# Kernel tuning notes

Hardware: AMD Instinct MI355X
Metric: run time of the kernel (lower is better)

## Reference

```python
import jax, jax.numpy as jnp
import numpy as np

DELTA = 0.1
LRELU_SLOPE = 0.01
BN_EPS = 1e-5


def ternarize(t, d):
    # {-1, 0, +1}: 0 where |t| < d, sign(t) otherwise (matches the torch where-chain)
    return jnp.where(jnp.abs(t) < d, 0.0, jnp.sign(t))


def ste_ternarize(t, d):
    # straight-through estimator, matching the torch .data-swap trick
    return t + jax.lax.stop_gradient(ternarize(t, d) - t)


def conv2d(x, w, stride, pad):
    return jax.lax.conv_general_dilated(
        x, w, (stride, stride), [(pad, pad), (pad, pad)],
        dimension_numbers=('NCHW', 'OIHW', 'NCHW'))


def batchnorm(x, gamma, beta, mean, var):
    inv = gamma / jnp.sqrt(var + BN_EPS)
    return x * inv[None, :, None, None] + (beta - mean * inv)[None, :, None, None]


def lrelu(x):
    return jnp.where(x > 0, x, LRELU_SLOPE * x)


def setup_inputs() -> dict:
    key = jax.random.key(0)
    ks = jax.random.split(key, 12)
    B, Cin, C, H, W = 16, 32, 64, 256, 256
    return {
        'x':      jax.random.normal(ks[0], (B, Cin, H, W), jnp.float32),
        'w11':    jax.random.normal(ks[1], (C, Cin, 3, 3), jnp.float32),
        'b11':    jax.random.normal(ks[2], (C,), jnp.float32),
        'w1':     jax.random.normal(ks[3], (C, Cin, 3, 3), jnp.float32),
        'b1':     jax.random.normal(ks[4], (C,), jnp.float32),
        'w2':     jax.random.normal(ks[5], (C, C, 3, 3), jnp.float32),
        'b2':     jax.random.normal(ks[6], (C,), jnp.float32),
        'gamma_p': jax.random.uniform(ks[7], (Cin,), jnp.float32),
        'beta_p':  jax.random.normal(ks[8], (Cin,), jnp.float32),
        'mean_p':  jax.random.normal(ks[9], (Cin,), jnp.float32),
        'var_p':   jnp.ones((Cin,), jnp.float32),
        'gamma1':  jax.random.uniform(ks[10], (C,), jnp.float32),
        'beta1':   jax.random.normal(ks[11], (C,), jnp.float32),
        'mean1':   jax.random.normal(jax.random.fold_in(key, 99), (C,), jnp.float32),
        'var1':    jnp.ones((C,), jnp.float32),
    }


def reference(x, w11, b11, w1, b1, w2, b2,
              gamma_p, beta_p, mean_p, var_p,
              gamma1, beta1, mean1, var1):
    # shortcut conv11 (stride 3); NOTE: torch mutates input.data in-place, so
    # the main branch below consumes the x already ternarized with d11.
    d11 = DELTA * jnp.max(jnp.abs(w11))
    x_t = ste_ternarize(x, d11)
    prev_mp = conv2d(x_t, ste_ternarize(w11, d11), 3, 1) \
        + ste_ternarize(b11, d11)[None, :, None, None]

    # main branch: pre_bn -> lrelu -> conv1 (stride 1) -> bn1 -> lrelu -> dropout(eval) -> conv2 (stride 3)
    out = lrelu(batchnorm(x_t, gamma_p, beta_p, mean_p, var_p))

    d1 = DELTA * jnp.max(jnp.abs(w1))
    out = conv2d(ste_ternarize(out, d1), ste_ternarize(w1, d1), 1, 1) \
        + ste_ternarize(b1, d1)[None, :, None, None]
    out = lrelu(batchnorm(out, gamma1, beta1, mean1, var1))
    # dropout: identity in eval mode

    d2 = DELTA * jnp.max(jnp.abs(w2))
    out = conv2d(ste_ternarize(out, d2), ste_ternarize(w2, d2), 3, 1) \
        + ste_ternarize(b2, d2)[None, :, None, None]

    return lrelu(out + prev_mp)  # [16, 64, 86, 86]
```

## Files before the change

kernel.cpp:

```cpp
#include <hip/hip_runtime.h>
#include <stdint.h>

#define B 16
#define CIN 32
#define C 64
#define H 256
#define W 256
#define OH 86
#define OW 86
#define PIX (OH*OW)
#define PADW 272
#define PWORDS (PADW*PADW*8)

typedef int v4i __attribute__((ext_vector_type(4)));

#define OFF_D      0
#define OFF_MAPW   64
#define OFF_B11    768
#define OFF_B2     1280
#define OFF_TLO    1536
#define OFF_THI    1792
#define OFF_W11R   4096
#define OFF_W1R    24576
#define OFF_W2R    45056
#define OFF_XTP    262144
#define OFF_XMAP   38141952

__device__ __forceinline__ int tern_i(float t, float d) {
    return (fabsf(t) < d) ? 0 : (t > 0.f ? 1 : -1);
}

__global__ __launch_bounds__(1024) void k_absmax(const float* w11, const float* w1,
                                                 const float* w2, unsigned* dws) {
    __shared__ unsigned red[1024];
    int b = blockIdx.x;
    const float* p = (b == 0) ? w11 : (b == 1) ? w1 : w2;
    int n = (b == 2) ? 36864 : 18432;
    unsigned m = 0;
    for (int i = threadIdx.x; i < n; i += 1024)
        m = max(m, __float_as_uint(fabsf(p[i])));
    red[threadIdx.x] = m; __syncthreads();
    for (int s = 512; s > 0; s >>= 1) {
        if (threadIdx.x < s) red[threadIdx.x] = max(red[threadIdx.x], red[threadIdx.x + s]);
        __syncthreads();
    }
    if (threadIdx.x == 0) dws[b] = red[0];
}

__global__ __launch_bounds__(256) void k_prep(const float* w11, const float* w1, const float* w2,
                                              const float* b11, const float* b1, const float* b2,
                                              const float* gp, const float* bp, const float* mp, const float* vp,
                                              const float* g1, const float* be1, const float* me1, const float* v1,
                                              char* ws) {
    const unsigned* dw = (const unsigned*)(ws + OFF_D);
    float d11 = __fmul_rn(0.1f, __uint_as_float(dw[0]));
    float d1  = __fmul_rn(0.1f, __uint_as_float(dw[1]));
    float d2v = __fmul_rn(0.1f, __uint_as_float(dw[2]));
    int idx = blockIdx.x * 256 + threadIdx.x;
    if (idx < 4608) {
        int j = idx & 3, c16 = (idx >> 2) & 15, cot = (idx >> 6) & 3;
        int q1 = (idx >> 8) & 1, pos = idx >> 9;
        int co = cot * 16 + c16;
        unsigned wd = 0;
        #pragma unroll
        for (int jj = 0; jj < 4; jj++) {
            int ci = q1 * 16 + j * 4 + jj;
            int tv = tern_i(w1[(co * 32 + ci) * 9 + pos], d1);
            wd |= ((unsigned)(tv & 255)) << (8 * jj);
        }
        ((int*)(ws + OFF_W1R))[idx] = (int)wd;
    } else if (idx < 9216) {
        int i2 = idx - 4608;
        int j = i2 & 3, c16 = (i2 >> 2) & 15, cot = (i2 >> 6) & 3;
        int q1 = (i2 >> 8) & 1, pos = i2 >> 9;
        int co = cot * 16 + c16;
        unsigned wd = 0;
        #pragma unroll
        for (int jj = 0; jj < 4; jj++) {
            int ci = q1 * 16 + j * 4 + jj;
            int tv = tern_i(w11[(co * 32 + ci) * 9 + pos], d11);
            wd |= ((unsigned)(tv & 255)) << (8 * jj);
        }
        ((int*)(ws + OFF_W11R))[i2] = (int)wd;
    } else if (idx < 18432) {
        int i2 = idx - 9216;
        int j = i2 & 3, q = (i2 >> 2) & 3, c16 = (i2 >> 4) & 15;
        int cot = (i2 >> 8) & 3, pos = i2 >> 10;
        int co = cot * 16 + c16;
        unsigned wd = 0;
        #pragma unroll
        for (int jj = 0; jj < 4; jj++) {
            int ci = q * 16 + j * 4 + jj;
            int tv = tern_i(w2[(co * 64 + ci) * 9 + pos], d2v);
            wd |= ((unsigned)(tv & 255)) << (8 * jj);
        }
        ((int*)(ws + OFF_W2R))[i2] = (int)wd;
    } else {
        int i = idx - 18432;
        if (i < 64) {
            ((int*)(ws + OFF_B11))[i] = tern_i(b11[i], d11);
        } else if (i < 128) {
            ((int*)(ws + OFF_B2))[i - 64] = tern_i(b2[i - 64], d2v);
        } else if (i < 152) {
            int j = i - 128;
            int g = j / 3, s = j % 3;
            float v = (float)(s - 1);
            unsigned wd = 0;
            #pragma unroll
            for (int jj = 0; jj < 4; jj++) {
                int c = g * 4 + jj;
                float inv = __fdiv_rn(gp[c], __fsqrt_rn(__fadd_rn(vp[c], 1e-5f)));
                float sh  = __fsub_rn(bp[c], __fmul_rn(mp[c], inv));
                float z   = __fadd_rn(__fmul_rn(v, inv), sh);
                z = (z > 0.f) ? z : __fmul_rn(0.01f, z);
                wd |= ((unsigned)(tern_i(z, d1) & 255)) << (8 * jj);
            }
            ((int*)(ws + OFF_MAPW))[j] = (int)wd;
        } else if (i < 216) {
            int co = i - 152;
            float inv = __fdiv_rn(g1[co], __fsqrt_rn(__fadd_rn(v1[co], 1e-5f)));
            float sh  = __fsub_rn(be1[co], __fmul_rn(me1[co], inv));
            int lo = 1000, hi = 1000;
            for (int vi = -290; vi <= 290; ++vi) {
                float z = __fadd_rn(__fmul_rn((float)vi, inv), sh);
                z = (z > 0.f) ? z : __fmul_rn(0.01f, z);
                int cls = (fabsf(z) < d2v) ? 0 : (z > 0.f ? 1 : -1);
                if (cls >= 0 && lo == 1000) lo = vi;
                if (cls == 1 && hi == 1000) hi = vi;
            }
            int b1t = tern_i(b1[co], d1);
            ((int*)(ws + OFF_TLO))[co] = lo - b1t;
            ((int*)(ws + OFF_THI))[co] = hi - b1t;
        }
    }
}

__global__ __launch_bounds__(256) void k_tern_x(const float* __restrict__ x,
                                                char* __restrict__ ws) {
    int bidx = blockIdx.x;
    if (bidx >= 4096) {
        int idx = (bidx - 4096) * 256 + threadIdx.x;
        int n = idx / 8448, c = idx - n * 8448;
        int row, col;
        if (c < 4352) {
            int r = c / 272; col = c - r * 272; row = (r < 2) ? r : r + 256;
        } else {
            int c2 = c - 4352; int k = c2 & 15;
            row = 2 + (c2 >> 4); col = (k < 2) ? k : k + 256;
        }
        size_t base = ((size_t)n * (PADW * PADW) + (size_t)row * PADW + col) * 2;
        int4 z = make_int4(0, 0, 0, 0);
        ((int4*)(ws + OFF_XTP))[base] = z;  ((int4*)(ws + OFF_XTP))[base + 1] = z;
        ((int4*)(ws + OFF_XMAP))[base] = z; ((int4*)(ws + OFF_XMAP))[base + 1] = z;
        return;
    }
    float d11 = __fmul_rn(0.1f, __uint_as_float(((const unsigned*)(ws + OFF_D))[0]));
    const int* mapw = (const int*)(ws + OFF_MAPW);
    int idx = bidx * 256 + threadIdx.x;
    int pix = idx & 65535, n = idx >> 16;
    int y = pix >> 8, xq = pix & 255;
    const float* xp = x + ((size_t)n * CIN << 16) + pix;
    int rw[8], mw[8];
    #pragma unroll
    for (int g = 0; g < 8; ++g) {
        unsigned Wn = (unsigned)mapw[g * 3 + 0];
        unsigned W0 = (unsigned)mapw[g * 3 + 1];
        unsigned Wp = (unsigned)mapw[g * 3 + 2];
        unsigned r = 0;
        #pragma unroll
        for (int j = 0; j < 4; ++j) {
            float v = xp[(size_t)(g * 4 + j) << 16];
            int tv = tern_i(v, d11);
            r |= ((unsigned)(tv & 255)) << (8 * j);
        }
        unsigned nb = (r & 0x80808080u) >> 7;
        unsigned pb = (r & 0x01010101u) & ~nb;
        unsigned nm = nb * 0xFFu, pm = pb * 0xFFu;
        unsigned zm = ~(nm | pm);
        rw[g] = (int)r;
        mw[g] = (int)((Wn & nm) | (W0 & zm) | (Wp & pm));
    }
    size_t base = ((size_t)n * (PADW * PADW) + (size_t)(y + 2) * PADW + (xq + 2)) * 2;
    int4* o1 = (int4*)(ws + OFF_XTP) + base;
    o1[0] = make_int4(rw[0], rw[1], rw[2], rw[3]);
    o1[1] = make_int4(rw[4], rw[5], rw[6], rw[7]);
    int4* o2 = (int4*)(ws + OFF_XMAP) + base;
    o2[0] = make_int4(mw[0], mw[1], mw[2], mw[3]);
    o2[1] = make_int4(mw[4], mw[5], mw[6], mw[7]);
}

__global__ __launch_bounds__(256, 3) void k_net(const char* __restrict__ ws,
                                                float* __restrict__ out) {
    __shared__ int t2L[576 * 16];
    int tid = threadIdx.x, bid = blockIdx.x;
    int tx = bid % 11; int tt = bid / 11; int ty = tt % 11; int n = tt / 11;
    int OH0 = ty * 8, OW0 = tx * 8;
    int Y0 = OH0 * 3 - 2, X0 = OW0 * 3 - 2;
    int c16 = tid & 15, q = (tid >> 4) & 3, wv = tid >> 6;
    int q1 = q & 1, qh = q >> 1;
    const int* xmapn = (const int*)(ws + OFF_XMAP) + (size_t)n * PWORDS;
    const int* xtpn  = (const int*)(ws + OFF_XTP)  + (size_t)n * PWORDS;

    const int* w1r = (const int*)(ws + OFF_W1R);
    v4i bw1[5][4];
    #pragma unroll
    for (int c = 0; c < 5; ++c) {
        int pos = 2 * c + qh;
        #pragma unroll
        for (int ct = 0; ct < 4; ++ct) {
            v4i z = {0, 0, 0, 0};
            if (pos < 9) z = *(const v4i*)&w1r[((pos * 2 + q1) * 4 + ct) * 64 + c16 * 4];
            bw1[c][ct] = z;
        }
    }
    const int* TLO = (const int*)(ws + OFF_TLO);
    const int* THI = (const int*)(ws + OFF_THI);
    v4i tlo4[4], thi4[4];
    #pragma unroll
    for (int ct = 0; ct < 4; ++ct) {
        tlo4[ct] = *(const v4i*)&TLO[ct * 16 + q * 4];
        thi4[ct] = *(const v4i*)&THI[ct * 16 + q * 4];
    }

    int Yb = Y0 + 2, Xb = X0 + 2;
    #pragma unroll 1
    for (int pg = 0; pg < 9; ++pg) {
        int pbase = (wv * 9 + pg) * 16;
        int fp = pbase + c16;
        int iy = fp / 24, ix = fp - iy * 24;
        v4i a[5];
        #pragma unroll
        for (int c = 0; c < 5; ++c) {
            int pos = 2 * c + qh;
            v4i z = {0, 0, 0, 0};
            if (pos < 9) {
                int kh = pos / 3, kw = pos - kh * 3;
                z = *(const v4i*)&xmapn[((Yb + iy + kh) * PADW + (Xb + ix + kw)) * 8 + q1 * 4];
            }
            a[c] = z;
        }
        bool wok = ((unsigned)(Y0 + 1 + iy) < H) && ((unsigned)(X0 + 1 + ix) < W);
        int key = (fp >> 1) & 3;
        #pragma unroll
        for (int ct = 0; ct < 4; ++ct) {
            v4i acc = {0, 0, 0, 0};
            #pragma unroll
            for (int c = 0; c < 5; ++c)
                acc = __builtin_amdgcn_mfma_i32_16x16x64_i8(bw1[c][ct], a[c], acc, 0, 0, 0);
            unsigned wcol = 0;
            #pragma unroll
            for (int i = 0; i < 4; ++i) {
                int cls = (acc[i] >= tlo4[ct][i] ? 1 : 0) + (acc[i] >= thi4[ct][i] ? 1 : 0) - 1;
                wcol |= ((unsigned)(cls & 255)) << (8 * i);
            }
            t2L[fp * 16 + ((ct ^ key) << 2) + q] = wok ? (int)wcol : 0;
        }
    }

    int o = wv * 16 + c16;
    int oh8 = o >> 3, ow8 = o & 7;
    int gOH = OH0 + oh8, gOW = OW0 + ow8;
    v4i a11[5];
    #pragma unroll
    for (int c = 0; c < 5; ++c) {
        int pos = 2 * c + qh;
        v4i z = {0, 0, 0, 0};
        if (pos < 9) {
            int kh = pos / 3, kw = pos - kh * 3;
            int ih = gOH * 3 - 1 + kh, iw = gOW * 3 - 1 + kw;
            z = *(const v4i*)&xtpn[((ih + 2) * PADW + (iw + 2)) * 8 + q1 * 4];
        }
        a11[c] = z;
    }
    const int* w11r = (const int*)(ws + OFF_W11R);
    v4i acc11[4];
    #pragma unroll
    for (int ct = 0; ct < 4; ++ct) {
        v4i acc1 = {0, 0, 0, 0};
        #pragma unroll
        for (int c = 0; c < 5; ++c) {
            int pos = 2 * c + qh;
            v4i b = {0, 0, 0, 0};
            if (pos < 9) b = *(const v4i*)&w11r[((pos * 2 + q1) * 4 + ct) * 64 + c16 * 4];
            acc1 = __builtin_amdgcn_mfma_i32_16x16x64_i8(a11[c], b, acc1, 0, 0, 0);
        }
        acc11[ct] = acc1;
    }
    __syncthreads();

    v4i a2[9];
    #pragma unroll
    for (int pos = 0; pos < 9; ++pos) {
        int kh = pos / 3, kw = pos - kh * 3;
        int p2 = (oh8 * 3 + kh) * 24 + ow8 * 3 + kw;
        int g2 = q ^ ((p2 >> 1) & 3);
        a2[pos] = *(const v4i*)&t2L[p2 * 16 + g2 * 4];
    }
    const int* w2r = (const int*)(ws + OFF_W2R);
    v4i acc2[4];
    #pragma unroll
    for (int ct = 0; ct < 4; ++ct) {
        v4i acc = {0, 0, 0, 0};
        #pragma unroll
        for (int pos = 0; pos < 9; ++pos) {
            v4i b = *(const v4i*)&w2r[((pos * 4 + ct) * 16 + c16) * 16 + q * 4];
            acc = __builtin_amdgcn_mfma_i32_16x16x64_i8(a2[pos], b, acc, 0, 0, 0);
        }
        acc2[ct] = acc;
    }

    const int* b2i = (const int*)(ws + OFF_B2);
    const int* b11i = (const int*)(ws + OFF_B11);
    int pt0 = wv * 16 + q * 4;
    int ohh = OH0 + (pt0 >> 3);
    int oww = OW0 + (pt0 & 7);
    if (ohh < OH) {
        #pragma unroll
        for (int ct = 0; ct < 4; ++ct) {
            int co = ct * 16 + c16;
            int bc = b2i[co] + b11i[co];
            float f[4];
            #pragma unroll
            for (int i = 0; i < 4; ++i) {
                float z = (float)(acc2[ct][i] + acc11[ct][i] + bc);
                f[i] = (z > 0.f) ? z : __fmul_rn(0.01f, z);
            }
            float* op = out + ((size_t)(n * 64 + co)) * PIX + ohh * OW + oww;
            if (oww + 3 < OW) {
                *(float4*)op = make_float4(f[0], f[1], f[2], f[3]);
            } else {
                #pragma unroll
                for (int i = 0; i < 4; ++i)
                    if (oww + i < OW) op[i] = f[i];
            }
        }
    }
}

extern "C" void kernel_launch(void* const* d_in, const int* in_sizes, int n_in,
                              void* d_out, int out_size, void* d_ws, size_t ws_size,
                              hipStream_t stream) {
    const float* x    = (const float*)d_in[0];
    const float* w11  = (const float*)d_in[1];
    const float* b11  = (const float*)d_in[2];
    const float* w1   = (const float*)d_in[3];
    const float* b1   = (const float*)d_in[4];
    const float* w2   = (const float*)d_in[5];
    const float* b2   = (const float*)d_in[6];
    const float* gp   = (const float*)d_in[7];
    const float* bp   = (const float*)d_in[8];
    const float* mp   = (const float*)d_in[9];
    const float* vp   = (const float*)d_in[10];
    const float* g1   = (const float*)d_in[11];
    const float* be1  = (const float*)d_in[12];
    const float* me1  = (const float*)d_in[13];
    const float* v1   = (const float*)d_in[14];
    char* ws = (char*)d_ws;
    float* out = (float*)d_out;

    k_absmax<<<3, 1024, 0, stream>>>(w11, w1, w2, (unsigned*)(ws + OFF_D));
    k_prep<<<73, 256, 0, stream>>>(w11, w1, w2, b11, b1, b2,
                                   gp, bp, mp, vp, g1, be1, me1, v1, ws);
    k_tern_x<<<4096 + 528, 256, 0, stream>>>(x, ws);
    k_net<<<11 * 11 * B, 256, 0, stream>>>(ws, out);
}
```

Measured before the change: 140.1 us.

## Fuse input ternarization into main kernel via shared-memory halo tiles

Removes the separate k_tern_x pass and its two padded int8 workspace images. Each k_net block now reads its 26x26 input halo straight from x, ternarizes it and builds the mapped tile in shared memory with a swizzled layout. The shortcut conv11 is moved ahead of conv1 so it can reuse the t2L buffer before that buffer is overwritten. This saves one kernel launch and a global write/read round trip, at the cost of recomputing overlapping halo pixels, more shared memory, and occupancy lowered to 2 blocks per SIMD.

```diff
diff --git a/kernel.cpp b/kernel.cpp
--- a/kernel.cpp
+++ b/kernel.cpp
@@ -9,8 +9,6 @@
 #define OH 86
 #define OW 86
 #define PIX (OH*OW)
-#define PADW 272
-#define PWORDS (PADW*PADW*8)
 
 typedef int v4i __attribute__((ext_vector_type(4)));
 
@@ -23,8 +21,6 @@
 #define OFF_W11R   4096
 #define OFF_W1R    24576
 #define OFF_W2R    45056
-#define OFF_XTP    262144
-#define OFF_XMAP   38141952
 
 __device__ __forceinline__ int tern_i(float t, float d) {
     return (fabsf(t) < d) ? 0 : (t > 0.f ? 1 : -1);
@@ -135,71 +131,82 @@
     }
 }
 
-__global__ __launch_bounds__(256) void k_tern_x(const float* __restrict__ x,
-                                                char* __restrict__ ws) {
-    int bidx = blockIdx.x;
-    if (bidx >= 4096) {
-        int idx = (bidx - 4096) * 256 + threadIdx.x;
-        int n = idx / 8448, c = idx - n * 8448;
-        int row, col;
-        if (c < 4352) {
-            int r = c / 272; col = c - r * 272; row = (r < 2) ? r : r + 256;
-        } else {
-            int c2 = c - 4352; int k = c2 & 15;
-            row = 2 + (c2 >> 4); col = (k < 2) ? k : k + 256;
-        }
-        size_t base = ((size_t)n * (PADW * PADW) + (size_t)row * PADW + col) * 2;
-        int4 z = make_int4(0, 0, 0, 0);
-        ((int4*)(ws + OFF_XTP))[base] = z;  ((int4*)(ws + OFF_XTP))[base + 1] = z;
-        ((int4*)(ws + OFF_XMAP))[base] = z; ((int4*)(ws + OFF_XMAP))[base + 1] = z;
-        return;
-    }
-    float d11 = __fmul_rn(0.1f, __uint_as_float(((const unsigned*)(ws + OFF_D))[0]));
-    const int* mapw = (const int*)(ws + OFF_MAPW);
-    int idx = bidx * 256 + threadIdx.x;
-    int pix = idx & 65535, n = idx >> 16;
-    int y = pix >> 8, xq = pix & 255;
-    const float* xp = x + ((size_t)n * CIN << 16) + pix;
-    int rw[8], mw[8];
-    #pragma unroll
-    for (int g = 0; g < 8; ++g) {
-        unsigned Wn = (unsigned)mapw[g * 3 + 0];
-        unsigned W0 = (unsigned)mapw[g * 3 + 1];
-        unsigned Wp = (unsigned)mapw[g * 3 + 2];
-        unsigned r = 0;
-        #pragma unroll
-        for (int j = 0; j < 4; ++j) {
-            float v = xp[(size_t)(g * 4 + j) << 16];
-            int tv = tern_i(v, d11);
-            r |= ((unsigned)(tv & 255)) << (8 * j);
-        }
-        unsigned nb = (r & 0x80808080u) >> 7;
-        unsigned pb = (r & 0x01010101u) & ~nb;
-        unsigned nm = nb * 0xFFu, pm = pb * 0xFFu;
-        unsigned zm = ~(nm | pm);
-        rw[g] = (int)r;
-        mw[g] = (int)((Wn & nm) | (W0 & zm) | (Wp & pm));
-    }
-    size_t base = ((size_t)n * (PADW * PADW) + (size_t)(y + 2) * PADW + (xq + 2)) * 2;
-    int4* o1 = (int4*)(ws + OFF_XTP) + base;
-    o1[0] = make_int4(rw[0], rw[1], rw[2], rw[3]);
-    o1[1] = make_int4(rw[4], rw[5], rw[6], rw[7]);
-    int4* o2 = (int4*)(ws + OFF_XMAP) + base;
-    o2[0] = make_int4(mw[0], mw[1], mw[2], mw[3]);
-    o2[1] = make_int4(mw[4], mw[5], mw[6], mw[7]);
-}
-
-__global__ __launch_bounds__(256, 3) void k_net(const char* __restrict__ ws,
+__global__ __launch_bounds__(256, 2) void k_net(const float* __restrict__ x,
+                                                const char* __restrict__ ws,
                                                 float* __restrict__ out) {
-    __shared__ int t2L[576 * 16];
+    __shared__ int t2L[9216];
+    __shared__ int mapL[5408];
     int tid = threadIdx.x, bid = blockIdx.x;
     int tx = bid % 11; int tt = bid / 11; int ty = tt % 11; int n = tt / 11;
     int OH0 = ty * 8, OW0 = tx * 8;
     int Y0 = OH0 * 3 - 2, X0 = OW0 * 3 - 2;
     int c16 = tid & 15, q = (tid >> 4) & 3, wv = tid >> 6;
     int q1 = q & 1, qh = q >> 1;
-    const int* xmapn = (const int*)(ws + OFF_XMAP) + (size_t)n * PWORDS;
-    const int* xtpn  = (const int*)(ws + OFF_XTP)  + (size_t)n * PWORDS;
+    const float* xn = x + ((size_t)n * CIN << 16);
+    float d11 = __fmul_rn(0.1f, __uint_as_float(((const unsigned*)(ws + OFF_D))[0]));
+    const int* mapw = (const int*)(ws + OFF_MAPW);
+
+    #pragma unroll
+    for (int g = 0; g < 8; ++g) {
+        unsigned Wn = (unsigned)mapw[g * 3 + 0];
+        unsigned W0 = (unsigned)mapw[g * 3 + 1];
+        unsigned Wp = (unsigned)mapw[g * 3 + 2];
+        for (int pix = tid; pix < 676; pix += 256) {
+            int my = pix / 26, mx = pix - my * 26;
+            int gy = Y0 + my, gx = X0 + mx;
+            unsigned r = 0, m = 0;
+            if ((unsigned)gy < H && (unsigned)gx < W) {
+                const float* xp = xn + ((size_t)(g * 4) << 16) + (gy << 8) + gx;
+                #pragma unroll
+                for (int j = 0; j < 4; ++j) {
+                    float v = xp[(size_t)j << 16];
+                    int tv = tern_i(v, d11);
+                    r |= ((unsigned)(tv & 255)) << (8 * j);
+                }
+                unsigned nb = (r & 0x80808080u) >> 7;
+                unsigned pb = (r & 0x01010101u) & ~nb;
+                unsigned nm = nb * 0xFFu, pm = pb * 0xFFu;
+                unsigned zm = ~(nm | pm);
+                m = (Wn & nm) | (W0 & zm) | (Wp & pm);
+            }
+            int hs = (g >> 2) ^ ((gx & 1) ^ ((gx >> 2) & 1));
+            t2L[pix * 8 + hs * 4 + (g & 3)] = (int)r;
+            mapL[pix * 8 + hs * 4 + (g & 3)] = (int)m;
+        }
+    }
+    __syncthreads();
+
+    int o = wv * 16 + c16;
+    int oh8 = o >> 3, ow8 = o & 7;
+    v4i a11[5];
+    #pragma unroll
+    for (int c = 0; c < 5; ++c) {
+        int pos = 2 * c + qh;
+        v4i z = {0, 0, 0, 0};
+        if (pos < 9) {
+            int kh = pos / 3, kw = pos - kh * 3;
+            int my = oh8 * 3 + kh + 1, mx = ow8 * 3 + kw + 1;
+            int gxl = X0 + mx;
+            int hb = q1 ^ ((gxl & 1) ^ ((gxl >> 2) & 1));
+            z = *(const v4i*)&t2L[(my * 26 + mx) * 8 + hb * 4];
+        }
+        a11[c] = z;
+    }
+    const int* w11r = (const int*)(ws + OFF_W11R);
+    v4i acc11[4];
+    #pragma unroll
+    for (int ct = 0; ct < 4; ++ct) {
+        v4i acc1 = {0, 0, 0, 0};
+        #pragma unroll
+        for (int c = 0; c < 5; ++c) {
+            int pos = 2 * c + qh;
+            v4i b = {0, 0, 0, 0};
+            if (pos < 9) b = *(const v4i*)&w11r[((pos * 2 + q1) * 4 + ct) * 64 + c16 * 4];
+            acc1 = __builtin_amdgcn_mfma_i32_16x16x64_i8(a11[c], b, acc1, 0, 0, 0);
+        }
+        acc11[ct] = acc1;
+    }
+    __syncthreads();
 
     const int* w1r = (const int*)(ws + OFF_W1R);
     v4i bw1[5][4];
@@ -221,8 +228,6 @@
         tlo4[ct] = *(const v4i*)&TLO[ct * 16 + q * 4];
         thi4[ct] = *(const v4i*)&THI[ct * 16 + q * 4];
     }
-
-    int Yb = Y0 + 2, Xb = X0 + 2;
     #pragma unroll 1
     for (int pg = 0; pg < 9; ++pg) {
         int pbase = (wv * 9 + pg) * 16;
@@ -235,7 +240,9 @@
             v4i z = {0, 0, 0, 0};
             if (pos < 9) {
                 int kh = pos / 3, kw = pos - kh * 3;
-                z = *(const v4i*)&xmapn[((Yb + iy + kh) * PADW + (Xb + ix + kw)) * 8 + q1 * 4];
+                int gxl = X0 + ix + kw;
+                int hb = q1 ^ ((gxl & 1) ^ ((gxl >> 2) & 1));
+                z = *(const v4i*)&mapL[((iy + kh) * 26 + (ix + kw)) * 8 + hb * 4];
             }
             a[c] = z;
         }
@@ -255,36 +262,6 @@
             }
             t2L[fp * 16 + ((ct ^ key) << 2) + q] = wok ? (int)wcol : 0;
         }
-    }
-
-    int o = wv * 16 + c16;
-    int oh8 = o >> 3, ow8 = o & 7;
-    int gOH = OH0 + oh8, gOW = OW0 + ow8;
-    v4i a11[5];
-    #pragma unroll
-    for (int c = 0; c < 5; ++c) {
-        int pos = 2 * c + qh;
-        v4i z = {0, 0, 0, 0};
-        if (pos < 9) {
-            int kh = pos / 3, kw = pos - kh * 3;
-            int ih = gOH * 3 - 1 + kh, iw = gOW * 3 - 1 + kw;
-            z = *(const v4i*)&xtpn[((ih + 2) * PADW + (iw + 2)) * 8 + q1 * 4];
-        }
-        a11[c] = z;
-    }
-    const int* w11r = (const int*)(ws + OFF_W11R);
-    v4i acc11[4];
-    #pragma unroll
-    for (int ct = 0; ct < 4; ++ct) {
-        v4i acc1 = {0, 0, 0, 0};
-        #pragma unroll
-        for (int c = 0; c < 5; ++c) {
-            int pos = 2 * c + qh;
-            v4i b = {0, 0, 0, 0};
-            if (pos < 9) b = *(const v4i*)&w11r[((pos * 2 + q1) * 4 + ct) * 64 + c16 * 4];
-            acc1 = __builtin_amdgcn_mfma_i32_16x16x64_i8(a11[c], b, acc1, 0, 0, 0);
-        }
-        acc11[ct] = acc1;
     }
     __syncthreads();
 
@@ -361,6 +338,5 @@
     k_absmax<<<3, 1024, 0, stream>>>(w11, w1, w2, (unsigned*)(ws + OFF_D));
     k_prep<<<73, 256, 0, stream>>>(w11, w1, w2, b11, b1, b2,
                                    gp, bp, mp, vp, g1, be1, me1, v1, ws);
-    k_tern_x<<<4096 + 528, 256, 0, stream>>>(x, ws);
-    k_net<<<11 * 11 * B, 256, 0, stream>>>(ws, out);
-}
+    k_net<<<11 * 11 * B, 256, 0, stream>>>(x, ws, out);
+}
```

Result: slower. 159.9 us (+14.1%).
